# Kernel tuning notes

Measured on AMD Instinct MI355X. Metric: run time of the kernel, lower is better.

## Reference

```python
import jax, jax.numpy as jnp
import numpy as np

B, N, F = 2, 2048, 64
H, C = 4, 32          # attention heads, channels per head
HID = 128             # hidden_size
HIN = H * C           # hidden_size_in = 128
MASK = -10e9          # spektral dense-GAT mask constant


def setup_inputs() -> dict:
    key = jax.random.key(0)
    ks = jax.random.split(key, 48)
    inp = {}
    inp['x'] = jax.random.normal(ks[0], (B, N, F), dtype=jnp.float32)
    adj = (jax.random.uniform(ks[1], (B, N, N)) < 0.03).astype(jnp.float32)
    inp['a'] = jnp.clip(adj + jnp.eye(N, dtype=jnp.float32)[None], 0.0, 1.0)
    inp['h_p'] = jax.random.normal(ks[2], (B, N, HID), dtype=jnp.float32) * 0.1
    inp['h_mu'] = jax.random.normal(ks[3], (B, N, HID), dtype=jnp.float32) * 0.1
    inp['h_sigma'] = jax.random.normal(ks[4], (B, N, HID), dtype=jnp.float32) * 0.1
    # GAT params
    inp['gat_kernel'] = jax.random.normal(ks[5], (F, H, C), dtype=jnp.float32) / np.float32(np.sqrt(F))
    inp['gat_attn_self'] = jax.random.normal(ks[6], (H, C), dtype=jnp.float32) * 0.1
    inp['gat_attn_neigh'] = jax.random.normal(ks[7], (H, C), dtype=jnp.float32) * 0.1
    inp['gat_bias'] = jnp.zeros((H * C,), dtype=jnp.float32)
    # GRU-style gate params for p / mu / sigma
    ki = 8
    for nm in ('p', 'mu', 'sigma'):
        for g in ('u', 'r', 'c'):
            inp[f'W_{g}_{nm}'] = jax.random.normal(ks[ki], (HID + HIN, HID), dtype=jnp.float32) / np.float32(np.sqrt(HID + HIN)); ki += 1
            inp[f'b_{g}_{nm}'] = jax.random.normal(ks[ki], (N, 1), dtype=jnp.float32) * 0.05; ki += 1
    # bilinear decoders
    for nm in ('p', 'mu', 'sigma'):
        inp[f'R_{nm}'] = jax.random.normal(ks[ki], (HID, HID), dtype=jnp.float32) / np.float32(np.sqrt(HID)); ki += 1
    return inp


def _gat(x, a, kernel, attn_self, attn_neigh, bias):
    # dense spektral GATConv, concat_heads=True, no activation
    h = jnp.einsum('bnf,fhc->bnhc', x, kernel)                 # [B,N,H,C]
    s_self = jnp.einsum('bnhc,hc->bnh', h, attn_self)          # [B,N,H]
    s_neigh = jnp.einsum('bnhc,hc->bnh', h, attn_neigh)        # [B,N,H]
    scores = s_self[:, :, None, :] + s_neigh[:, None, :, :]    # [B,N,N,H]
    scores = jax.nn.leaky_relu(scores, negative_slope=0.2)
    scores = scores + MASK * (1.0 - a)[..., None]
    attn = jax.nn.softmax(scores, axis=2)                      # softmax over neighbors j
    out = jnp.einsum('bijh,bjhc->bihc', attn, h)               # [B,N,H,C]
    return out.reshape(out.shape[0], out.shape[1], H * C) + bias


def _gru(conv, h, Wu, Wr, Wc, bu, br, bc):
    ch = jnp.concatenate([conv, h], axis=-1)                   # [B,N,HIN+HID]
    u = jax.nn.sigmoid(bu + ch @ Wu)                           # bias [N,1] broadcasts
    r = jax.nn.sigmoid(br + ch @ Wr)
    c = jnp.tanh(bc + jnp.concatenate([conv, r * h], axis=-1) @ Wc)
    return u * h + (1.0 - u) * c


def _bilinear(h, R):
    return jnp.einsum('bnh,hk,bmk->bnm', h, R, h)              # x R x^T


def reference(x, a, h_p, h_mu, h_sigma,
              gat_kernel, gat_attn_self, gat_attn_neigh, gat_bias,
              W_u_p, b_u_p, W_r_p, b_r_p, W_c_p, b_c_p,
              W_u_mu, b_u_mu, W_r_mu, b_r_mu, W_c_mu, b_c_mu,
              W_u_sigma, b_u_sigma, W_r_sigma, b_r_sigma, W_c_sigma, b_c_sigma,
              R_p, R_mu, R_sigma):
    conv = _gat(x, a, gat_kernel, gat_attn_self, gat_attn_neigh, gat_bias)
    hp = _gru(conv, h_p, W_u_p, W_r_p, W_c_p, b_u_p, b_r_p, b_c_p)
    hmu = _gru(conv, h_mu, W_u_mu, W_r_mu, W_c_mu, b_u_mu, b_r_mu, b_c_mu)
    hsg = _gru(conv, h_sigma, W_u_sigma, W_r_sigma, W_c_sigma, b_u_sigma, b_r_sigma, b_c_sigma)
    p = _bilinear(hp, R_p)
    mu = _bilinear(hmu, R_mu)
    sigma = _bilinear(hsg, R_sigma)
    logits = jnp.stack([p, mu, sigma], axis=-1)                # [B,N,N,3]
    return logits, hp, hmu, hsg
```

## Files before the change

kernel.cpp:

```cpp
#include <hip/hip_runtime.h>
#include <hip/hip_bf16.h>

typedef __attribute__((ext_vector_type(4))) float f32x4;
typedef __attribute__((ext_vector_type(8))) short bf16x8;

static constexpr int B   = 2;
static constexpr int N   = 2048;
static constexpr int F   = 64;
static constexpr int H   = 4;
static constexpr int HID = 128;
static constexpr int BN  = B * N;
static constexpr size_t LOG_SZ = (size_t)B * N * N * 3;

__device__ __forceinline__ float sigmoidf_(float x) { return 1.0f / (1.0f + __expf(-x)); }
__device__ __forceinline__ float tanhf_(float x) {
  float e = __expf(2.0f * x);
  return 1.0f - 2.0f / (e + 1.0f);
}
__device__ __forceinline__ void split_bf16(float v, short& hi, short& lo) {
  unsigned u = __float_as_uint(v);
  unsigned hr = (u + 0x7FFFu + ((u >> 16) & 1u)) >> 16;
  hi = (short)hr;
  float hv = __uint_as_float(hr << 16);
  float res = v - hv;
  unsigned u2 = __float_as_uint(res);
  lo = (short)((u2 + 0x7FFFu + ((u2 >> 16) & 1u)) >> 16);
}

__device__ __forceinline__ void stage16(const short* gp, short* lp) {
  __builtin_amdgcn_global_load_lds(
      (const __attribute__((address_space(1))) void*)gp,
      (__attribute__((address_space(3))) void*)lp, 16, 0, 0);
}

struct PreArgs {
  const float* x; const float* gk; const float* asel; const float* anei;
  float* hfeat; float* sself; float* sneigh;
  const float* h[3];
  short* hh[3]; short* hl[3];
  const float* src[12];
  short* whi[12]; short* wlo[12];
  int nks[12];
};
__global__ __launch_bounds__(256) void k_pre(PreArgs pa) {
  const int bid = blockIdx.x;
  if (bid < BN / 2) {
    const int t = threadIdx.x;
    const int r = t >> 7, tt = t & 127;
    const int bn = bid * 2 + r;
    __shared__ float xs[2][F];
    if (tt < F) xs[r][tt] = pa.x[(size_t)bn * F + tt];
    const size_t o = (size_t)bn * HID + tt;
    { short hi, lo; split_bf16(pa.h[0][o], hi, lo); pa.hh[0][o] = hi; pa.hl[0][o] = lo; }
    { short hi, lo; split_bf16(pa.h[1][o], hi, lo); pa.hh[1][o] = hi; pa.hl[1][o] = lo; }
    { short hi, lo; split_bf16(pa.h[2][o], hi, lo); pa.hh[2][o] = hi; pa.hl[2][o] = lo; }
    __syncthreads();
    float acc = 0.f;
    #pragma unroll 8
    for (int f = 0; f < F; ++f) acc += xs[r][f] * pa.gk[f * HID + tt];
    pa.hfeat[o] = acc;
    float ps = acc * pa.asel[tt];
    float pn = acc * pa.anei[tt];
    #pragma unroll
    for (int d = 16; d >= 1; d >>= 1) {
      ps += __shfl_xor(ps, d, 32);
      pn += __shfl_xor(pn, d, 32);
    }
    if ((tt & 31) == 0) {
      pa.sself [bn * H + (tt >> 5)] = ps;
      pa.sneigh[bn * H + (tt >> 5)] = pn;
    }
  } else {
    const int pb = bid - BN / 2;
    const int m = pb >> 3, cf = pb & 7;
    const int nksv = pa.nks[m];
    const int wv = threadIdx.x >> 6, lane = threadIdx.x & 63;
    const float* src = pa.src[m];
    short* ph = pa.whi[m];
    short* pl = pa.wlo[m];
    const int col = cf * 16 + (lane & 15);
    const int krow = (lane >> 4) * 8;
    for (int ks = wv; ks < nksv; ks += 4) {
      bf16x8 vh, vl;
      #pragma unroll
      for (int e = 0; e < 8; ++e) {
        const int k = ks * 32 + krow + e;
        short hi, lo; split_bf16(src[(size_t)k * HID + col], hi, lo);
        vh[e] = hi; vl[e] = lo;
      }
      const size_t o = (((size_t)cf * nksv + ks) * 64 + lane) * 8;
      *(bf16x8*)&ph[o] = vh;
      *(bf16x8*)&pl[o] = vl;
    }
  }
}

__global__ __launch_bounds__(256) void k_attn(
    const float* __restrict__ a, const float* __restrict__ hfeat,
    const float* __restrict__ sself, const float* __restrict__ sneigh,
    const float* __restrict__ bias,
    short* __restrict__ conv_hi, short* __restrict__ conv_lo) {
  const int wv   = threadIdx.x >> 6;
  const int lane = threadIdx.x & 63;
  const int bi   = blockIdx.x * 4 + wv;
  const int bbase = bi & ~(N - 1);
  __shared__ int   nbr[4][256];
  __shared__ float wts[4][256][4];
  int*   nb       = nbr[wv];
  float (*wt)[4]  = wts[wv];

  const float si0 = sself[bi * H + 0];
  const float si1 = sself[bi * H + 1];
  const float si2 = sself[bi * H + 2];
  const float si3 = sself[bi * H + 3];
  float den0 = 0.f, den1 = 0.f, den2 = 0.f, den3 = 0.f;
  float acc0 = 0.f, acc1 = 0.f;
  const unsigned long long lmlt = ((unsigned long long)1 << lane) - 1ull;
  const float* arow = a + (size_t)bi * N;
  const float* hb   = hfeat + (size_t)bbase * HID;
  const float* snb  = sneigh + (size_t)bbase * H;
  const int h0 = lane >> 5;
  int num = 0;

  auto flush = [&]() {
    asm volatile("s_waitcnt lgkmcnt(0)" ::: "memory");
    for (int n = lane; n < num; n += 64) {
      const int j = nb[n];
      f32x4 sn = *(const f32x4*)&snb[(size_t)j * H];
      float s0 = si0 + sn[0]; s0 = (s0 > 0.f) ? s0 : 0.2f * s0;
      float s1 = si1 + sn[1]; s1 = (s1 > 0.f) ? s1 : 0.2f * s1;
      float s2 = si2 + sn[2]; s2 = (s2 > 0.f) ? s2 : 0.2f * s2;
      float s3 = si3 + sn[3]; s3 = (s3 > 0.f) ? s3 : 0.2f * s3;
      float w0 = __expf(s0), w1 = __expf(s1), w2 = __expf(s2), w3 = __expf(s3);
      wt[n][0] = w0; wt[n][1] = w1; wt[n][2] = w2; wt[n][3] = w3;
      den0 += w0; den1 += w1; den2 += w2; den3 += w3;
    }
    asm volatile("s_waitcnt lgkmcnt(0)" ::: "memory");
    #pragma unroll 4
    for (int n = 0; n < num; ++n) {
      const int j  = nb[n];
      const float wA = wt[n][h0];
      const float wB = wt[n][h0 + 2];
      const float* hr = hb + (size_t)j * HID;
      acc0 += wA * hr[lane];
      acc1 += wB * hr[lane + 64];
    }
    asm volatile("s_waitcnt lgkmcnt(0)" ::: "memory");
    num = 0;
  };

  for (int jb = 0; jb < N; jb += 256) {
    f32x4 av = *(const f32x4*)&arow[jb + lane * 4];
    #pragma unroll
    for (int e = 0; e < 4; ++e) {
      const unsigned long long m = __ballot(av[e] > 0.5f);
      if (av[e] > 0.5f) {
        const int pos = num + __popcll(m & lmlt);
        nb[pos] = jb + lane * 4 + e;
      }
      num += __popcll(m);
      if (num > 192) flush();
    }
  }
  if (num > 0) flush();

  #pragma unroll
  for (int d = 32; d >= 1; d >>= 1) {
    den0 += __shfl_xor(den0, d, 64);
    den1 += __shfl_xor(den1, d, 64);
    den2 += __shfl_xor(den2, d, 64);
    den3 += __shfl_xor(den3, d, 64);
  }
  const float dA = h0 ? den1 : den0;
  const float dB = h0 ? den3 : den2;
  const float v0 = acc0 / dA + bias[lane];
  const float v1 = acc1 / dB + bias[64 + lane];
  { short hi, lo; split_bf16(v0, hi, lo);
    conv_hi[(size_t)bi * HID + lane] = hi; conv_lo[(size_t)bi * HID + lane] = lo; }
  { short hi, lo; split_bf16(v1, hi, lo);
    conv_hi[(size_t)bi * HID + 64 + lane] = hi; conv_lo[(size_t)bi * HID + 64 + lane] = lo; }
}

struct GArgs {
  const short* chi; const short* clo;
  const float* h[3];
  const short* hhi[3]; const short* hlo[3];
  const float* bu[3]; const float* br[3]; const float* bc[3];
  const short* WuH[3]; const short* WuL[3];
  const short* WrH[3]; const short* WrL[3];
  const short* WcH[3]; const short* WcL[3];
  const short* RtH[3]; const short* RtL[3];
  float* u_ws[3];
  short* rhh[3]; short* rhl[3];
  short* hph[3]; short* hpl[3];
  float* hout[3]; __hip_bfloat16* hb[3]; __hip_bfloat16* gb[3];
};

__global__ __launch_bounds__(256) void k_ur(GArgs ga) {
  const int wv = threadIdx.x >> 6, lane = threadIdx.x & 63;
  const int bx = blockIdx.x, cg = blockIdx.y;
  const int gate = blockIdx.z & 1, cell = blockIdx.z >> 1;
  const int lr = lane & 15, lg = lane >> 4, kb = lg * 8;
  const int R0 = bx * 64 + wv * 16;
  __shared__ short wlds[2][16][64][8];

  bf16x8 a_h[8], a_l[8];
  {
    const size_t ab = (size_t)(R0 + lr) * HID + kb;
    const short* hhi = ga.hhi[cell]; const short* hlo = ga.hlo[cell];
    #pragma unroll
    for (int ks = 0; ks < 4; ++ks) {
      a_h[ks]     = *(const bf16x8*)&ga.chi[ab + ks * 32];
      a_l[ks]     = *(const bf16x8*)&ga.clo[ab + ks * 32];
      a_h[4 + ks] = *(const bf16x8*)&hhi[ab + ks * 32];
      a_l[4 + ks] = *(const bf16x8*)&hlo[ab + ks * 32];
    }
  }
  {
    const short* WH = gate ? ga.WrH[cell] : ga.WuH[cell];
    const short* WL = gate ? ga.WrL[cell] : ga.WuL[cell];
    #pragma unroll
    for (int i = 0; i < 8; ++i) {
      const int fid = wv * 8 + i;
      const int combo = fid >> 4, f = fid & 15;
      const short* src = combo ? WL : WH;
      const short* gp = src + (((size_t)((cg * 2 + (f >> 3)) * 8 + (f & 7))) * 64 + lane) * 8;
      stage16(gp, &wlds[combo][f][0][0]);
    }
  }
  asm volatile("s_waitcnt vmcnt(0)" ::: "memory");
  __syncthreads();

  f32x4 acc[2] = {};
  #pragma unroll
  for (int ks = 0; ks < 8; ++ks) {
    const bf16x8 ah = a_h[ks], al = a_l[ks];
    #pragma unroll
    for (int cfl = 0; cfl < 2; ++cfl) {
      const int f = cfl * 8 + ks;
      bf16x8 bh = *(const bf16x8*)&wlds[0][f][lane][0];
      bf16x8 bl = *(const bf16x8*)&wlds[1][f][lane][0];
      acc[cfl] = __builtin_amdgcn_mfma_f32_16x16x32_bf16(ah, bh, acc[cfl], 0, 0, 0);
      acc[cfl] = __builtin_amdgcn_mfma_f32_16x16x32_bf16(ah, bl, acc[cfl], 0, 0, 0);
      acc[cfl] = __builtin_amdgcn_mfma_f32_16x16x32_bf16(al, bh, acc[cfl], 0, 0, 0);
    }
  }
  if (gate == 0) {
    const float* bu = ga.bu[cell];
    float* uws = ga.u_ws[cell];
    #pragma unroll
    for (int cfl = 0; cfl < 2; ++cfl) {
      const int col = cg * 32 + cfl * 16 + lr;
      #pragma unroll
      for (int q = 0; q < 4; ++q) {
        const int row = R0 + lg * 4 + q;
        uws[(size_t)row * HID + col] = sigmoidf_(acc[cfl][q] + bu[row & (N - 1)]);
      }
    }
  } else {
    const float* br = ga.br[cell];
    const float* hsrc = ga.h[cell];
    short* rhh = ga.rhh[cell]; short* rhl = ga.rhl[cell];
    #pragma unroll
    for (int cfl = 0; cfl < 2; ++cfl) {
      const int col = cg * 32 + cfl * 16 + lr;
      #pragma unroll
      for (int q = 0; q < 4; ++q) {
        const int row = R0 + lg * 4 + q;
        const float rv = sigmoidf_(acc[cfl][q] + br[row & (N - 1)]);
        const float rhv = rv * hsrc[(size_t)row * HID + col];
        short hi, lo; split_bf16(rhv, hi, lo);
        rhh[(size_t)row * HID + col] = hi;
        rhl[(size_t)row * HID + col] = lo;
      }
    }
  }
}

__global__ __launch_bounds__(256) void k_c(GArgs ga) {
  const int wv = threadIdx.x >> 6, lane = threadIdx.x & 63;
  const int bx = blockIdx.x, cg = blockIdx.y, cell = blockIdx.z;
  const int lr = lane & 15, lg = lane >> 4, kb = lg * 8;
  const int R0 = bx * 64 + wv * 16;
  __shared__ short wlds[2][16][64][8];

  bf16x8 a_h[8], a_l[8];
  {
    const size_t ab = (size_t)(R0 + lr) * HID + kb;
    const short* rhh = ga.rhh[cell]; const short* rhl = ga.rhl[cell];
    #pragma unroll
    for (int ks = 0; ks < 4; ++ks) {
      a_h[ks]     = *(const bf16x8*)&ga.chi[ab + ks * 32];
      a_l[ks]     = *(const bf16x8*)&ga.clo[ab + ks * 32];
      a_h[4 + ks] = *(const bf16x8*)&rhh[ab + ks * 32];
      a_l[4 + ks] = *(const bf16x8*)&rhl[ab + ks * 32];
    }
  }
  {
    const short* WH = ga.WcH[cell];
    const short* WL = ga.WcL[cell];
    #pragma unroll
    for (int i = 0; i < 8; ++i) {
      const int fid = wv * 8 + i;
      const int combo = fid >> 4, f = fid & 15;
      const short* src = combo ? WL : WH;
      const short* gp = src + (((size_t)((cg * 2 + (f >> 3)) * 8 + (f & 7))) * 64 + lane) * 8;
      stage16(gp, &wlds[combo][f][0][0]);
    }
  }
  asm volatile("s_waitcnt vmcnt(0)" ::: "memory");
  __syncthreads();

  f32x4 acc[2] = {};
  #pragma unroll
  for (int ks = 0; ks < 8; ++ks) {
    const bf16x8 ah = a_h[ks], al = a_l[ks];
    #pragma unroll
    for (int cfl = 0; cfl < 2; ++cfl) {
      const int f = cfl * 8 + ks;
      bf16x8 bh = *(const bf16x8*)&wlds[0][f][lane][0];
      bf16x8 bl = *(const bf16x8*)&wlds[1][f][lane][0];
      acc[cfl] = __builtin_amdgcn_mfma_f32_16x16x32_bf16(ah, bh, acc[cfl], 0, 0, 0);
      acc[cfl] = __builtin_amdgcn_mfma_f32_16x16x32_bf16(ah, bl, acc[cfl], 0, 0, 0);
      acc[cfl] = __builtin_amdgcn_mfma_f32_16x16x32_bf16(al, bh, acc[cfl], 0, 0, 0);
    }
  }
  const float* bc = ga.bc[cell];
  const float* uw = ga.u_ws[cell];
  const float* hsrc = ga.h[cell];
  float* hout = ga.hout[cell];
  __hip_bfloat16* hbo = ga.hb[cell];
  short* hph = ga.hph[cell]; short* hpl = ga.hpl[cell];
  #pragma unroll
  for (int cfl = 0; cfl < 2; ++cfl) {
    const int col = cg * 32 + cfl * 16 + lr;
    #pragma unroll
    for (int q = 0; q < 4; ++q) {
      const int row = R0 + lg * 4 + q;
      const float cv = tanhf_(acc[cfl][q] + bc[row & (N - 1)]);
      const float uv = uw[(size_t)row * HID + col];
      const float hv = hsrc[(size_t)row * HID + col];
      const float o = uv * hv + (1.f - uv) * cv;
      hout[(size_t)row * HID + col] = o;
      hbo[(size_t)row * HID + col] = __float2bfloat16(o);
      short hi, lo; split_bf16(o, hi, lo);
      hph[(size_t)row * HID + col] = hi;
      hpl[(size_t)row * HID + col] = lo;
    }
  }
}

__global__ __launch_bounds__(256) void k_g(GArgs ga) {
  const int wv = threadIdx.x >> 6, lane = threadIdx.x & 63;
  const int bx = blockIdx.x, cg = blockIdx.y, cell = blockIdx.z;
  const int lr = lane & 15, lg = lane >> 4, kb = lg * 8;
  const int R0 = bx * 64 + wv * 16;
  __shared__ short wlds[2][8][64][8];

  bf16x8 a_h[4], a_l[4];
  {
    const size_t ab = (size_t)(R0 + lr) * HID + kb;
    const short* hph = ga.hph[cell]; const short* hpl = ga.hpl[cell];
    #pragma unroll
    for (int ks = 0; ks < 4; ++ks) {
      a_h[ks] = *(const bf16x8*)&hph[ab + ks * 32];
      a_l[ks] = *(const bf16x8*)&hpl[ab + ks * 32];
    }
  }
  {
    #pragma unroll
    for (int i = 0; i < 4; ++i) {
      const int fid = wv * 4 + i;
      const int combo = fid >> 3, f = fid & 7;
      const short* src = combo ? ga.RtL[cell] : ga.RtH[cell];
      const short* gp = src + (((size_t)((cg * 2 + (f >> 2)) * 4 + (f & 3))) * 64 + lane) * 8;
      stage16(gp, &wlds[combo][f][0][0]);
    }
  }
  asm volatile("s_waitcnt vmcnt(0)" ::: "memory");
  __syncthreads();

  f32x4 acc[2] = {};
  #pragma unroll
  for (int ks = 0; ks < 4; ++ks) {
    const bf16x8 ah = a_h[ks], al = a_l[ks];
    #pragma unroll
    for (int cfl = 0; cfl < 2; ++cfl) {
      const int f = cfl * 4 + ks;
      bf16x8 bh = *(const bf16x8*)&wlds[0][f][lane][0];
      bf16x8 bl = *(const bf16x8*)&wlds[1][f][lane][0];
      acc[cfl] = __builtin_amdgcn_mfma_f32_16x16x32_bf16(ah, bh, acc[cfl], 0, 0, 0);
      acc[cfl] = __builtin_amdgcn_mfma_f32_16x16x32_bf16(ah, bl, acc[cfl], 0, 0, 0);
      acc[cfl] = __builtin_amdgcn_mfma_f32_16x16x32_bf16(al, bh, acc[cfl], 0, 0, 0);
    }
  }
  __hip_bfloat16* gbo = ga.gb[cell];
  #pragma unroll
  for (int cfl = 0; cfl < 2; ++cfl) {
    const int col = cg * 32 + cfl * 16 + lr;
    #pragma unroll
    for (int q = 0; q < 4; ++q) {
      const int row = R0 + lg * 4 + q;
      gbo[(size_t)row * HID + col] = __float2bfloat16(acc[cfl][q]);
    }
  }
}

__global__ __launch_bounds__(256) void k_bilinear(
    const __hip_bfloat16* __restrict__ g0, const __hip_bfloat16* __restrict__ g1,
    const __hip_bfloat16* __restrict__ g2, const __hip_bfloat16* __restrict__ h0,
    const __hip_bfloat16* __restrict__ h1, const __hip_bfloat16* __restrict__ h2,
    float* __restrict__ out) {
  const int ti = blockIdx.x, tj = blockIdx.y, b = blockIdx.z;
  const int t = threadIdx.x;
  const int w = t >> 6, l = t & 63;
  const int wi = w >> 1, wj = w & 1;
  const int i_base = ti * 64 + wi * 32;
  const int j_base = tj * 64 + wj * 32;
  const __hip_bfloat16* gbs[3] = {g0, g1, g2};
  const __hip_bfloat16* hbs[3] = {h0, h1, h2};
  const int lr = l & 15;
  const int kb = (l >> 4) * 8;
  f32x4 acc[3][2][2] = {};
  for (int k0 = 0; k0 < HID; k0 += 32) {
    bf16x8 af[3][2], bfr[3][2];
    #pragma unroll
    for (int d = 0; d < 3; ++d) {
      #pragma unroll
      for (int m = 0; m < 2; ++m) {
        af[d][m]  = *(const bf16x8*)&gbs[d][(size_t)(b * N + i_base + m * 16 + lr) * HID + k0 + kb];
        bfr[d][m] = *(const bf16x8*)&hbs[d][(size_t)(b * N + j_base + m * 16 + lr) * HID + k0 + kb];
      }
    }
    #pragma unroll
    for (int d = 0; d < 3; ++d)
      #pragma unroll
      for (int mi = 0; mi < 2; ++mi)
        #pragma unroll
        for (int mj = 0; mj < 2; ++mj)
          acc[d][mi][mj] = __builtin_amdgcn_mfma_f32_16x16x32_bf16(
              af[d][mi], bfr[d][mj], acc[d][mi][mj], 0, 0, 0);
  }
  const int orow = (l >> 4) * 4;
  const int col  = l & 15;
  #pragma unroll
  for (int mi = 0; mi < 2; ++mi)
    #pragma unroll
    for (int mj = 0; mj < 2; ++mj)
      #pragma unroll
      for (int r = 0; r < 4; ++r) {
        const int row = i_base + mi * 16 + orow + r;
        const int cc  = j_base + mj * 16 + col;
        float* p = &out[(((size_t)(b * N + row)) * N + cc) * 3];
        p[0] = acc[0][mi][mj][r];
        p[1] = acc[1][mi][mj][r];
        p[2] = acc[2][mi][mj][r];
      }
}

extern "C" void kernel_launch(void* const* d_in, const int* in_sizes, int n_in,
                              void* d_out, int out_size, void* d_ws, size_t ws_size,
                              hipStream_t stream) {
  (void)in_sizes; (void)n_in; (void)out_size; (void)ws_size;
  const float* a    = (const float*)d_in[1];
  const float* bias = (const float*)d_in[8];

  float* ws      = (float*)d_ws;
  float* hfeat   = ws;
  float* sself   = hfeat + (size_t)BN * HID;
  float* sneigh  = sself + (size_t)BN * H;
  float* u_ws0   = sneigh + (size_t)BN * H;
  short* sp      = (short*)(u_ws0 + 3 * (size_t)BN * HID);
  auto alloc_s = [&](size_t n) { short* p = sp; sp += n; return p; };

  short* conv_hi = alloc_s((size_t)BN * HID);
  short* conv_lo = alloc_s((size_t)BN * HID);
  short* h_hi[3]; short* h_lo[3];
  for (int c = 0; c < 3; ++c) { h_hi[c] = alloc_s((size_t)BN * HID); h_lo[c] = alloc_s((size_t)BN * HID); }
  short* rh_hi[3]; short* rh_lo[3];
  for (int c = 0; c < 3; ++c) { rh_hi[c] = alloc_s((size_t)BN * HID); rh_lo[c] = alloc_s((size_t)BN * HID); }
  short* hp_hi[3]; short* hp_lo[3];
  for (int c = 0; c < 3; ++c) { hp_hi[c] = alloc_s((size_t)BN * HID); hp_lo[c] = alloc_s((size_t)BN * HID); }
  __hip_bfloat16* hbb[3]; __hip_bfloat16* gbb[3];
  for (int c = 0; c < 3; ++c) {
    hbb[c] = (__hip_bfloat16*)alloc_s((size_t)BN * HID);
    gbb[c] = (__hip_bfloat16*)alloc_s((size_t)BN * HID);
  }

  float* out = (float*)d_out;

  PreArgs pa;
  pa.x = (const float*)d_in[0];
  pa.gk = (const float*)d_in[5];
  pa.asel = (const float*)d_in[6];
  pa.anei = (const float*)d_in[7];
  pa.hfeat = hfeat; pa.sself = sself; pa.sneigh = sneigh;

  GArgs ga;
  ga.chi = conv_hi; ga.clo = conv_lo;
  ga.h[0] = (const float*)d_in[2];
  ga.h[1] = (const float*)d_in[3];
  ga.h[2] = (const float*)d_in[4];
  for (int c = 0; c < 3; ++c) {
    pa.h[c] = ga.h[c];
    pa.hh[c] = h_hi[c]; pa.hl[c] = h_lo[c];
    const int base = 9 + c * 6;
    ga.hhi[c] = h_hi[c]; ga.hlo[c] = h_lo[c];
    ga.bu[c] = (const float*)d_in[base + 1];
    ga.br[c] = (const float*)d_in[base + 3];
    ga.bc[c] = (const float*)d_in[base + 5];
    short* wu_h = alloc_s(256 * 128); short* wu_l = alloc_s(256 * 128);
    short* wr_h = alloc_s(256 * 128); short* wr_l = alloc_s(256 * 128);
    short* wc_h = alloc_s(256 * 128); short* wc_l = alloc_s(256 * 128);
    short* rt_h = alloc_s(128 * 128); short* rt_l = alloc_s(128 * 128);
    const int pb = c * 4;
    pa.src[pb + 0] = (const float*)d_in[base + 0]; pa.whi[pb + 0] = wu_h; pa.wlo[pb + 0] = wu_l; pa.nks[pb + 0] = 8;
    pa.src[pb + 1] = (const float*)d_in[base + 2]; pa.whi[pb + 1] = wr_h; pa.wlo[pb + 1] = wr_l; pa.nks[pb + 1] = 8;
    pa.src[pb + 2] = (const float*)d_in[base + 4]; pa.whi[pb + 2] = wc_h; pa.wlo[pb + 2] = wc_l; pa.nks[pb + 2] = 8;
    pa.src[pb + 3] = (const float*)d_in[27 + c];   pa.whi[pb + 3] = rt_h; pa.wlo[pb + 3] = rt_l; pa.nks[pb + 3] = 4;
    ga.WuH[c] = wu_h; ga.WuL[c] = wu_l;
    ga.WrH[c] = wr_h; ga.WrL[c] = wr_l;
    ga.WcH[c] = wc_h; ga.WcL[c] = wc_l;
    ga.RtH[c] = rt_h; ga.RtL[c] = rt_l;
    ga.u_ws[c] = u_ws0 + (size_t)c * BN * HID;
    ga.rhh[c] = rh_hi[c]; ga.rhl[c] = rh_lo[c];
    ga.hph[c] = hp_hi[c]; ga.hpl[c] = hp_lo[c];
    ga.hout[c] = out + LOG_SZ + (size_t)c * BN * HID;
    ga.hb[c] = hbb[c];
    ga.gb[c] = gbb[c];
  }

  k_pre<<<BN / 2 + 96, 256, 0, stream>>>(pa);
  k_attn<<<BN / 4, 256, 0, stream>>>(a, hfeat, sself, sneigh, bias, conv_hi, conv_lo);
  k_ur<<<dim3(BN / 64, 4, 6), 256, 0, stream>>>(ga);
  k_c<<<dim3(BN / 64, 4, 3), 256, 0, stream>>>(ga);
  k_g<<<dim3(BN / 64, 4, 3), 256, 0, stream>>>(ga);
  dim3 g2(N / 64, N / 64, B);
  k_bilinear<<<g2, 256, 0, stream>>>(gbb[0], gbb[1], gbb[2],
                                     hbb[0], hbb[1], hbb[2], out);
}
```

Baseline: 116.3 us.

## Fuse all stages into one cooperative persistent megakernel with grid syncs

```diff
diff --git a/kernel.cpp b/kernel.cpp
--- a/kernel.cpp
+++ b/kernel.cpp
@@ -1,5 +1,8 @@
 #include <hip/hip_runtime.h>
 #include <hip/hip_bf16.h>
+#include <hip/hip_cooperative_groups.h>
+
+namespace cg = cooperative_groups;
 
 typedef __attribute__((ext_vector_type(4))) float f32x4;
 typedef __attribute__((ext_vector_type(8))) short bf16x8;
@@ -26,11 +29,428 @@
   unsigned u2 = __float_as_uint(res);
   lo = (short)((u2 + 0x7FFFu + ((u2 >> 16) & 1u)) >> 16);
 }
-
 __device__ __forceinline__ void stage16(const short* gp, short* lp) {
   __builtin_amdgcn_global_load_lds(
       (const __attribute__((address_space(1))) void*)gp,
       (__attribute__((address_space(3))) void*)lp, 16, 0, 0);
+}
+
+struct MegaArgs {
+  const float* x; const float* gk; const float* asel; const float* anei;
+  const float* a; const float* bias;
+  float* hfeat; float* sself; float* sneigh;
+  const float* h[3];
+  short* hh[3]; short* hl[3];
+  const float* wsrc[12];
+  short* whi[12]; short* wlo[12];
+  short* conv_hi; short* conv_lo;
+  const float* bu[3]; const float* br[3]; const float* bc[3];
+  const short* WuH[3]; const short* WuL[3];
+  const short* WrH[3]; const short* WrL[3];
+  const short* WcH[3]; const short* WcL[3];
+  const short* RtH[3]; const short* RtL[3];
+  float* u_ws[3];
+  short* rhh[3]; short* rhl[3];
+  short* hph[3]; short* hpl[3];
+  float* hout[3];
+  short* gb[3];
+  float* out;
+};
+
+__global__ __launch_bounds__(512, 4) void k_mega(MegaArgs A) {
+  cg::grid_group grid = cg::this_grid();
+  const int blk = blockIdx.x;
+  const int G   = gridDim.x;
+  const int t   = threadIdx.x;
+  const int wv  = t >> 6, lane = t & 63;
+  __shared__ char smem[65536];
+
+  {
+    float (*xs)[64] = (float (*)[64])smem;
+    const int sub = t >> 7, tt = t & 127;
+    for (int r0 = blk * 4; r0 < BN; r0 += G * 4) {
+      const int r = r0 + sub;
+      if (tt < 64) xs[sub][tt] = A.x[(size_t)r * F + tt];
+      const size_t o = (size_t)r * HID + tt;
+      { short hi, lo; split_bf16(A.h[0][o], hi, lo); A.hh[0][o] = hi; A.hl[0][o] = lo; }
+      { short hi, lo; split_bf16(A.h[1][o], hi, lo); A.hh[1][o] = hi; A.hl[1][o] = lo; }
+      { short hi, lo; split_bf16(A.h[2][o], hi, lo); A.hh[2][o] = hi; A.hl[2][o] = lo; }
+      __syncthreads();
+      float acc = 0.f;
+      #pragma unroll 8
+      for (int f = 0; f < F; ++f) acc += xs[sub][f] * A.gk[f * HID + tt];
+      A.hfeat[o] = acc;
+      float ps = acc * A.asel[tt];
+      float pn = acc * A.anei[tt];
+      #pragma unroll
+      for (int d = 16; d >= 1; d >>= 1) {
+        ps += __shfl_xor(ps, d, 32);
+        pn += __shfl_xor(pn, d, 32);
+      }
+      if ((tt & 31) == 0) {
+        A.sself [r * H + (tt >> 5)] = ps;
+        A.sneigh[r * H + (tt >> 5)] = pn;
+      }
+      __syncthreads();
+    }
+    for (int u = blk * 8 + wv; u < 672; u += G * 8) {
+      const int c = u / 224, rem = u % 224;
+      int m, cf, ks, nks;
+      if (rem < 192) { m = c * 4 + rem / 64; const int f2 = rem & 63; cf = f2 >> 3; ks = f2 & 7; nks = 8; }
+      else           { m = c * 4 + 3;        const int f2 = rem - 192; cf = f2 >> 2; ks = f2 & 3; nks = 4; }
+      const float* src = A.wsrc[m];
+      short* ph = A.whi[m];
+      short* pl = A.wlo[m];
+      const int col  = cf * 16 + (lane & 15);
+      const int krow = (lane >> 4) * 8;
+      bf16x8 vh, vl;
+      #pragma unroll
+      for (int e = 0; e < 8; ++e) {
+        short hi, lo; split_bf16(src[(size_t)(ks * 32 + krow + e) * HID + col], hi, lo);
+        vh[e] = hi; vl[e] = lo;
+      }
+      const size_t o = (((size_t)cf * nks + ks) * 64 + lane) * 8;
+      *(bf16x8*)&ph[o] = vh;
+      *(bf16x8*)&pl[o] = vl;
+    }
+  }
+  grid.sync();
+
+  {
+    int   (*nbrA)[256]    = (int (*)[256])smem;
+    float (*wtsA)[256][4] = (float (*)[256][4])(smem + 8192);
+    const unsigned long long lmlt = ((unsigned long long)1 << lane) - 1ull;
+    const int h0 = lane >> 5;
+    for (int bi = blk * 8 + wv; bi < BN; bi += G * 8) {
+      int*   nb      = nbrA[wv];
+      float (*wt)[4] = wtsA[wv];
+      const int bbase = bi & ~(N - 1);
+      const float si0 = A.sself[bi * H + 0];
+      const float si1 = A.sself[bi * H + 1];
+      const float si2 = A.sself[bi * H + 2];
+      const float si3 = A.sself[bi * H + 3];
+      float den0 = 0.f, den1 = 0.f, den2 = 0.f, den3 = 0.f;
+      float acc0 = 0.f, acc1 = 0.f;
+      const float* arow = A.a + (size_t)bi * N;
+      const float* hb   = A.hfeat + (size_t)bbase * HID;
+      const float* snb  = A.sneigh + (size_t)bbase * H;
+      int num = 0;
+
+      auto flush = [&]() {
+        asm volatile("s_waitcnt lgkmcnt(0)" ::: "memory");
+        for (int n = lane; n < num; n += 64) {
+          const int j = nb[n];
+          f32x4 sn = *(const f32x4*)&snb[(size_t)j * H];
+          float s0 = si0 + sn[0]; s0 = (s0 > 0.f) ? s0 : 0.2f * s0;
+          float s1 = si1 + sn[1]; s1 = (s1 > 0.f) ? s1 : 0.2f * s1;
+          float s2 = si2 + sn[2]; s2 = (s2 > 0.f) ? s2 : 0.2f * s2;
+          float s3 = si3 + sn[3]; s3 = (s3 > 0.f) ? s3 : 0.2f * s3;
+          float w0 = __expf(s0), w1 = __expf(s1), w2 = __expf(s2), w3 = __expf(s3);
+          wt[n][0] = w0; wt[n][1] = w1; wt[n][2] = w2; wt[n][3] = w3;
+          den0 += w0; den1 += w1; den2 += w2; den3 += w3;
+        }
+        asm volatile("s_waitcnt lgkmcnt(0)" ::: "memory");
+        #pragma unroll 4
+        for (int n = 0; n < num; ++n) {
+          const int j  = nb[n];
+          const float wA = wt[n][h0];
+          const float wB = wt[n][h0 + 2];
+          const float* hr = hb + (size_t)j * HID;
+          acc0 += wA * hr[lane];
+          acc1 += wB * hr[lane + 64];
+        }
+        asm volatile("s_waitcnt lgkmcnt(0)" ::: "memory");
+        num = 0;
+      };
+
+      for (int jb = 0; jb < N; jb += 256) {
+        f32x4 av = *(const f32x4*)&arow[jb + lane * 4];
+        #pragma unroll
+        for (int e = 0; e < 4; ++e) {
+          const unsigned long long m = __ballot(av[e] > 0.5f);
+          if (av[e] > 0.5f) {
+            const int pos = num + __popcll(m & lmlt);
+            nb[pos] = jb + lane * 4 + e;
+          }
+          num += __popcll(m);
+          if (num > 192) flush();
+        }
+      }
+      if (num > 0) flush();
+
+      #pragma unroll
+      for (int d = 32; d >= 1; d >>= 1) {
+        den0 += __shfl_xor(den0, d, 64);
+        den1 += __shfl_xor(den1, d, 64);
+        den2 += __shfl_xor(den2, d, 64);
+        den3 += __shfl_xor(den3, d, 64);
+      }
+      const float dA = h0 ? den1 : den0;
+      const float dB = h0 ? den3 : den2;
+      const float v0 = acc0 / dA + A.bias[lane];
+      const float v1 = acc1 / dB + A.bias[64 + lane];
+      { short hi, lo; split_bf16(v0, hi, lo);
+        A.conv_hi[(size_t)bi * HID + lane] = hi; A.conv_lo[(size_t)bi * HID + lane] = lo; }
+      { short hi, lo; split_bf16(v1, hi, lo);
+        A.conv_hi[(size_t)bi * HID + 64 + lane] = hi; A.conv_lo[(size_t)bi * HID + 64 + lane] = lo; }
+    }
+  }
+  grid.sync();
+
+  {
+    short (*wlds)[16][64][8] = (short (*)[16][64][8])smem;
+    const int lr = lane & 15, lg = lane >> 4, kb = lg * 8;
+    for (int vb = blk; vb < 384; vb += G) {
+      const int cell = vb >> 7, rem = vb & 127;
+      const int cgp = rem & 3, rb = rem >> 2;
+      const int R0 = rb * 128 + wv * 16;
+      bf16x8 a_h[8], a_l[8];
+      {
+        const size_t ab = (size_t)(R0 + lr) * HID + kb;
+        const short* hhi = A.hh[cell]; const short* hlo = A.hl[cell];
+        #pragma unroll
+        for (int ks = 0; ks < 4; ++ks) {
+          a_h[ks]     = *(const bf16x8*)&A.conv_hi[ab + ks * 32];
+          a_l[ks]     = *(const bf16x8*)&A.conv_lo[ab + ks * 32];
+          a_h[4 + ks] = *(const bf16x8*)&hhi[ab + ks * 32];
+          a_l[4 + ks] = *(const bf16x8*)&hlo[ab + ks * 32];
+        }
+      }
+      {
+        const short* srcs[4] = { A.WuH[cell], A.WuL[cell], A.WrH[cell], A.WrL[cell] };
+        #pragma unroll
+        for (int i = 0; i < 8; ++i) {
+          const int fid = wv * 8 + i;
+          const int combo = fid >> 4, f = fid & 15;
+          const short* gp = srcs[combo] +
+              (((size_t)((cgp * 2 + (f >> 3)) * 8 + (f & 7))) * 64 + lane) * 8;
+          stage16(gp, &wlds[combo][f][0][0]);
+        }
+      }
+      asm volatile("s_waitcnt vmcnt(0)" ::: "memory");
+      __syncthreads();
+
+      f32x4 au[2] = {}, ar[2] = {};
+      #pragma unroll
+      for (int ks = 0; ks < 8; ++ks) {
+        const bf16x8 ah = a_h[ks], al = a_l[ks];
+        #pragma unroll
+        for (int cfl = 0; cfl < 2; ++cfl) {
+          const int f = cfl * 8 + ks;
+          bf16x8 buh = *(const bf16x8*)&wlds[0][f][lane][0];
+          bf16x8 bul = *(const bf16x8*)&wlds[1][f][lane][0];
+          bf16x8 brh = *(const bf16x8*)&wlds[2][f][lane][0];
+          bf16x8 brl = *(const bf16x8*)&wlds[3][f][lane][0];
+          au[cfl] = __builtin_amdgcn_mfma_f32_16x16x32_bf16(ah, buh, au[cfl], 0, 0, 0);
+          au[cfl] = __builtin_amdgcn_mfma_f32_16x16x32_bf16(ah, bul, au[cfl], 0, 0, 0);
+          au[cfl] = __builtin_amdgcn_mfma_f32_16x16x32_bf16(al, buh, au[cfl], 0, 0, 0);
+          ar[cfl] = __builtin_amdgcn_mfma_f32_16x16x32_bf16(ah, brh, ar[cfl], 0, 0, 0);
+          ar[cfl] = __builtin_amdgcn_mfma_f32_16x16x32_bf16(ah, brl, ar[cfl], 0, 0, 0);
+          ar[cfl] = __builtin_amdgcn_mfma_f32_16x16x32_bf16(al, brh, ar[cfl], 0, 0, 0);
+        }
+      }
+      const float* bu = A.bu[cell];
+      const float* br = A.br[cell];
+      const float* hsrc = A.h[cell];
+      float* uws = A.u_ws[cell];
+      short* rhh = A.rhh[cell]; short* rhl = A.rhl[cell];
+      #pragma unroll
+      for (int cfl = 0; cfl < 2; ++cfl) {
+        const int col = cgp * 32 + cfl * 16 + lr;
+        #pragma unroll
+        for (int q = 0; q < 4; ++q) {
+          const int row = R0 + lg * 4 + q;
+          const int n = row & (N - 1);
+          uws[(size_t)row * HID + col] = sigmoidf_(au[cfl][q] + bu[n]);
+          const float rv = sigmoidf_(ar[cfl][q] + br[n]);
+          const float rhv = rv * hsrc[(size_t)row * HID + col];
+          short hi, lo; split_bf16(rhv, hi, lo);
+          rhh[(size_t)row * HID + col] = hi;
+          rhl[(size_t)row * HID + col] = lo;
+        }
+      }
+      __syncthreads();
+    }
+  }
+  grid.sync();
+
+  {
+    short (*wlds)[16][64][8] = (short (*)[16][64][8])smem;
+    const int lr = lane & 15, lg = lane >> 4, kb = lg * 8;
+    for (int vb = blk; vb < 384; vb += G) {
+      const int cell = vb >> 7, rem = vb & 127;
+      const int cgp = rem & 3, rb = rem >> 2;
+      const int R0 = rb * 128 + wv * 16;
+      bf16x8 a_h[8], a_l[8];
+      {
+        const size_t ab = (size_t)(R0 + lr) * HID + kb;
+        const short* rhh = A.rhh[cell]; const short* rhl = A.rhl[cell];
+        #pragma unroll
+        for (int ks = 0; ks < 4; ++ks) {
+          a_h[ks]     = *(const bf16x8*)&A.conv_hi[ab + ks * 32];
+          a_l[ks]     = *(const bf16x8*)&A.conv_lo[ab + ks * 32];
+          a_h[4 + ks] = *(const bf16x8*)&rhh[ab + ks * 32];
+          a_l[4 + ks] = *(const bf16x8*)&rhl[ab + ks * 32];
+        }
+      }
+      {
+        const short* srcs[2] = { A.WcH[cell], A.WcL[cell] };
+        #pragma unroll
+        for (int i = 0; i < 4; ++i) {
+          const int fid = wv * 4 + i;
+          const int combo = fid >> 4, f = fid & 15;
+          const short* gp = srcs[combo] +
+              (((size_t)((cgp * 2 + (f >> 3)) * 8 + (f & 7))) * 64 + lane) * 8;
+          stage16(gp, &wlds[combo][f][0][0]);
+        }
+      }
+      asm volatile("s_waitcnt vmcnt(0)" ::: "memory");
+      __syncthreads();
+
+      f32x4 acc[2] = {};
+      #pragma unroll
+      for (int ks = 0; ks < 8; ++ks) {
+        const bf16x8 ah = a_h[ks], al = a_l[ks];
+        #pragma unroll
+        for (int cfl = 0; cfl < 2; ++cfl) {
+          const int f = cfl * 8 + ks;
+          bf16x8 bh = *(const bf16x8*)&wlds[0][f][lane][0];
+          bf16x8 bl = *(const bf16x8*)&wlds[1][f][lane][0];
+          acc[cfl] = __builtin_amdgcn_mfma_f32_16x16x32_bf16(ah, bh, acc[cfl], 0, 0, 0);
+          acc[cfl] = __builtin_amdgcn_mfma_f32_16x16x32_bf16(ah, bl, acc[cfl], 0, 0, 0);
+          acc[cfl] = __builtin_amdgcn_mfma_f32_16x16x32_bf16(al, bh, acc[cfl], 0, 0, 0);
+        }
+      }
+      const float* bc = A.bc[cell];
+      const float* uw = A.u_ws[cell];
+      const float* hsrc = A.h[cell];
+      float* hout = A.hout[cell];
+      short* hph = A.hph[cell]; short* hpl = A.hpl[cell];
+      #pragma unroll
+      for (int cfl = 0; cfl < 2; ++cfl) {
+        const int col = cgp * 32 + cfl * 16 + lr;
+        #pragma unroll
+        for (int q = 0; q < 4; ++q) {
+          const int row = R0 + lg * 4 + q;
+          const float cv = tanhf_(acc[cfl][q] + bc[row & (N - 1)]);
+          const float uv = uw[(size_t)row * HID + col];
+          const float hv = hsrc[(size_t)row * HID + col];
+          const float o = uv * hv + (1.f - uv) * cv;
+          __builtin_nontemporal_store(o, &hout[(size_t)row * HID + col]);
+          short hi, lo; split_bf16(o, hi, lo);
+          hph[(size_t)row * HID + col] = hi;
+          hpl[(size_t)row * HID + col] = lo;
+        }
+      }
+      __syncthreads();
+    }
+  }
+  grid.sync();
+
+  {
+    short (*wlds)[8][64][8] = (short (*)[8][64][8])smem;
+    const int lr = lane & 15, lg = lane >> 4, kb = lg * 8;
+    for (int vb = blk; vb < 384; vb += G) {
+      const int cell = vb >> 7, rem = vb & 127;
+      const int cgp = rem & 3, rb = rem >> 2;
+      const int R0 = rb * 128 + wv * 16;
+      bf16x8 a_h[4], a_l[4];
+      {
+        const size_t ab = (size_t)(R0 + lr) * HID + kb;
+        const short* hph = A.hph[cell]; const short* hpl = A.hpl[cell];
+        #pragma unroll
+        for (int ks = 0; ks < 4; ++ks) {
+          a_h[ks] = *(const bf16x8*)&hph[ab + ks * 32];
+          a_l[ks] = *(const bf16x8*)&hpl[ab + ks * 32];
+        }
+      }
+      {
+        const short* srcs[2] = { A.RtH[cell], A.RtL[cell] };
+        #pragma unroll
+        for (int i = 0; i < 2; ++i) {
+          const int fid = wv * 2 + i;
+          const int combo = fid >> 3, f = fid & 7;
+          const short* gp = srcs[combo] +
+              (((size_t)((cgp * 2 + (f >> 2)) * 4 + (f & 3))) * 64 + lane) * 8;
+          stage16(gp, &wlds[combo][f][0][0]);
+        }
+      }
+      asm volatile("s_waitcnt vmcnt(0)" ::: "memory");
+      __syncthreads();
+
+      f32x4 acc[2] = {};
+      #pragma unroll
+      for (int ks = 0; ks < 4; ++ks) {
+        const bf16x8 ah = a_h[ks], al = a_l[ks];
+        #pragma unroll
+        for (int cfl = 0; cfl < 2; ++cfl) {
+          const int f = cfl * 4 + ks;
+          bf16x8 bh = *(const bf16x8*)&wlds[0][f][lane][0];
+          bf16x8 bl = *(const bf16x8*)&wlds[1][f][lane][0];
+          acc[cfl] = __builtin_amdgcn_mfma_f32_16x16x32_bf16(ah, bh, acc[cfl], 0, 0, 0);
+          acc[cfl] = __builtin_amdgcn_mfma_f32_16x16x32_bf16(ah, bl, acc[cfl], 0, 0, 0);
+          acc[cfl] = __builtin_amdgcn_mfma_f32_16x16x32_bf16(al, bh, acc[cfl], 0, 0, 0);
+        }
+      }
+      short* gbo = A.gb[cell];
+      #pragma unroll
+      for (int cfl = 0; cfl < 2; ++cfl) {
+        const int col = cgp * 32 + cfl * 16 + lr;
+        #pragma unroll
+        for (int q = 0; q < 4; ++q) {
+          const int row = R0 + lg * 4 + q;
+          short hi, lo; split_bf16(acc[cfl][q], hi, lo);
+          gbo[(size_t)row * HID + col] = hi;
+        }
+      }
+      __syncthreads();
+    }
+  }
+  grid.sync();
+
+  {
+    const int wi = wv >> 1, wj = wv & 1;
+    const int lr = lane & 15;
+    const int kb = (lane >> 4) * 8;
+    for (int u = blk; u < 1024; u += G) {
+      const int b = u >> 9, r = u & 511;
+      const int id2 = (r & 7) * 64 + (r >> 3);
+      const int ti = id2 & 15, tj = id2 >> 4;
+      const int i_base = ti * 128 + wi * 32;
+      const int j_base = tj * 64 + wj * 32;
+      f32x4 acc[3][2][2] = {};
+      for (int k0 = 0; k0 < HID; k0 += 32) {
+        #pragma unroll
+        for (int d = 0; d < 3; ++d) {
+          const short* gsrc = A.gb[d];
+          const short* hsrc = A.hph[d];
+          bf16x8 af0 = *(const bf16x8*)&gsrc[(size_t)(b * N + i_base + lr) * HID + k0 + kb];
+          bf16x8 af1 = *(const bf16x8*)&gsrc[(size_t)(b * N + i_base + 16 + lr) * HID + k0 + kb];
+          bf16x8 bf0 = *(const bf16x8*)&hsrc[(size_t)(b * N + j_base + lr) * HID + k0 + kb];
+          bf16x8 bf1 = *(const bf16x8*)&hsrc[(size_t)(b * N + j_base + 16 + lr) * HID + k0 + kb];
+          acc[d][0][0] = __builtin_amdgcn_mfma_f32_16x16x32_bf16(af0, bf0, acc[d][0][0], 0, 0, 0);
+          acc[d][0][1] = __builtin_amdgcn_mfma_f32_16x16x32_bf16(af0, bf1, acc[d][0][1], 0, 0, 0);
+          acc[d][1][0] = __builtin_amdgcn_mfma_f32_16x16x32_bf16(af1, bf0, acc[d][1][0], 0, 0, 0);
+          acc[d][1][1] = __builtin_amdgcn_mfma_f32_16x16x32_bf16(af1, bf1, acc[d][1][1], 0, 0, 0);
+        }
+      }
+      const int orow = (lane >> 4) * 4;
+      const int col  = lane & 15;
+      #pragma unroll
+      for (int mi = 0; mi < 2; ++mi)
+        #pragma unroll
+        for (int mj = 0; mj < 2; ++mj)
+          #pragma unroll
+          for (int rr = 0; rr < 4; ++rr) {
+            const int row = i_base + mi * 16 + orow + rr;
+            const int cc  = j_base + mj * 16 + col;
+            float* p = &A.out[(((size_t)(b * N + row)) * N + cc) * 3];
+            __builtin_nontemporal_store(acc[0][mi][mj][rr], p + 0);
+            __builtin_nontemporal_store(acc[1][mi][mj][rr], p + 1);
+            __builtin_nontemporal_store(acc[2][mi][mj][rr], p + 2);
+          }
+    }
+  }
 }
 
 struct PreArgs {
@@ -108,7 +528,6 @@
   __shared__ float wts[4][256][4];
   int*   nb       = nbr[wv];
   float (*wt)[4]  = wts[wv];
-
   const float si0 = sself[bi * H + 0];
   const float si1 = sself[bi * H + 1];
   const float si2 = sself[bi * H + 2];
@@ -121,7 +540,6 @@
   const float* snb  = sneigh + (size_t)bbase * H;
   const int h0 = lane >> 5;
   int num = 0;
-
   auto flush = [&]() {
     asm volatile("s_waitcnt lgkmcnt(0)" ::: "memory");
     for (int n = lane; n < num; n += 64) {
@@ -148,7 +566,6 @@
     asm volatile("s_waitcnt lgkmcnt(0)" ::: "memory");
     num = 0;
   };
-
   for (int jb = 0; jb < N; jb += 256) {
     f32x4 av = *(const f32x4*)&arow[jb + lane * 4];
     #pragma unroll
@@ -163,7 +580,6 @@
     }
   }
   if (num > 0) flush();
-
   #pragma unroll
   for (int d = 32; d >= 1; d >>= 1) {
     den0 += __shfl_xor(den0, d, 64);
@@ -193,17 +609,15 @@
   float* u_ws[3];
   short* rhh[3]; short* rhl[3];
   short* hph[3]; short* hpl[3];
-  float* hout[3]; __hip_bfloat16* hb[3]; __hip_bfloat16* gb[3];
+  float* hout[3]; short* gb[3];
 };
 
 __global__ __launch_bounds__(256) void k_ur(GArgs ga) {
   const int wv = threadIdx.x >> 6, lane = threadIdx.x & 63;
-  const int bx = blockIdx.x, cg = blockIdx.y;
-  const int gate = blockIdx.z & 1, cell = blockIdx.z >> 1;
+  const int bx = blockIdx.x, cg2 = blockIdx.y, cell = blockIdx.z;
   const int lr = lane & 15, lg = lane >> 4, kb = lg * 8;
   const int R0 = bx * 64 + wv * 16;
-  __shared__ short wlds[2][16][64][8];
-
+  __shared__ short wlds[4][16][64][8];
   bf16x8 a_h[8], a_l[8];
   {
     const size_t ab = (size_t)(R0 + lr) * HID + kb;
@@ -217,20 +631,89 @@
     }
   }
   {
-    const short* WH = gate ? ga.WrH[cell] : ga.WuH[cell];
-    const short* WL = gate ? ga.WrL[cell] : ga.WuL[cell];
+    const short* srcs[4] = { ga.WuH[cell], ga.WuL[cell], ga.WrH[cell], ga.WrL[cell] };
+    const short* sp = srcs[wv];
+    #pragma unroll
+    for (int f = 0; f < 16; ++f) {
+      const short* gp = sp + (((size_t)((cg2 * 2 + (f >> 3)) * 8 + (f & 7))) * 64 + lane) * 8;
+      stage16(gp, &wlds[wv][f][0][0]);
+    }
+  }
+  asm volatile("s_waitcnt vmcnt(0)" ::: "memory");
+  __syncthreads();
+  f32x4 au[2] = {}, ar[2] = {};
+  #pragma unroll
+  for (int ks = 0; ks < 8; ++ks) {
+    const bf16x8 ah = a_h[ks], al = a_l[ks];
+    #pragma unroll
+    for (int cfl = 0; cfl < 2; ++cfl) {
+      const int f = cfl * 8 + ks;
+      bf16x8 buh = *(const bf16x8*)&wlds[0][f][lane][0];
+      bf16x8 bul = *(const bf16x8*)&wlds[1][f][lane][0];
+      bf16x8 brh = *(const bf16x8*)&wlds[2][f][lane][0];
+      bf16x8 brl = *(const bf16x8*)&wlds[3][f][lane][0];
+      au[cfl] = __builtin_amdgcn_mfma_f32_16x16x32_bf16(ah, buh, au[cfl], 0, 0, 0);
+      au[cfl] = __builtin_amdgcn_mfma_f32_16x16x32_bf16(ah, bul, au[cfl], 0, 0, 0);
+      au[cfl] = __builtin_amdgcn_mfma_f32_16x16x32_bf16(al, buh, au[cfl], 0, 0, 0);
+      ar[cfl] = __builtin_amdgcn_mfma_f32_16x16x32_bf16(ah, brh, ar[cfl], 0, 0, 0);
+      ar[cfl] = __builtin_amdgcn_mfma_f32_16x16x32_bf16(ah, brl, ar[cfl], 0, 0, 0);
+      ar[cfl] = __builtin_amdgcn_mfma_f32_16x16x32_bf16(al, brh, ar[cfl], 0, 0, 0);
+    }
+  }
+  const float* bu = ga.bu[cell];
+  const float* br = ga.br[cell];
+  const float* hsrc = ga.h[cell];
+  float* uws = ga.u_ws[cell];
+  short* rhh = ga.rhh[cell]; short* rhl = ga.rhl[cell];
+  #pragma unroll
+  for (int cfl = 0; cfl < 2; ++cfl) {
+    const int col = cg2 * 32 + cfl * 16 + lr;
+    #pragma unroll
+    for (int q = 0; q < 4; ++q) {
+      const int row = R0 + lg * 4 + q;
+      const int n = row & (N - 1);
+      uws[(size_t)row * HID + col] = sigmoidf_(au[cfl][q] + bu[n]);
+      const float rv = sigmoidf_(ar[cfl][q] + br[n]);
+      const float rhv = rv * hsrc[(size_t)row * HID + col];
+      short hi, lo; split_bf16(rhv, hi, lo);
+      rhh[(size_t)row * HID + col] = hi;
+      rhl[(size_t)row * HID + col] = lo;
+    }
+  }
+}
+
+__global__ __launch_bounds__(256) void k_c(GArgs ga) {
+  const int wv = threadIdx.x >> 6, lane = threadIdx.x & 63;
+  const int bx = blockIdx.x, cg2 = blockIdx.y, cell = blockIdx.z;
+  const int lr = lane & 15, lg = lane >> 4, kb = lg * 8;
+  const int R0 = bx * 64 + wv * 16;
+  __shared__ short wlds[2][16][64][8];
+  bf16x8 a_h[8], a_l[8];
+  {
+    const size_t ab = (size_t)(R0 + lr) * HID + kb;
+    const short* rhh = ga.rhh[cell]; const short* rhl = ga.rhl[cell];
+    #pragma unroll
+    for (int ks = 0; ks < 4; ++ks) {
+      a_h[ks]     = *(const bf16x8*)&ga.chi[ab + ks * 32];
+      a_l[ks]     = *(const bf16x8*)&ga.clo[ab + ks * 32];
+      a_h[4 + ks] = *(const bf16x8*)&rhh[ab + ks * 32];
+      a_l[4 + ks] = *(const bf16x8*)&rhl[ab + ks * 32];
+    }
+  }
+  {
+    const short* WH = ga.WcH[cell];
+    const short* WL = ga.WcL[cell];
     #pragma unroll
     for (int i = 0; i < 8; ++i) {
       const int fid = wv * 8 + i;
       const int combo = fid >> 4, f = fid & 15;
       const short* src = combo ? WL : WH;
-      const short* gp = src + (((size_t)((cg * 2 + (f >> 3)) * 8 + (f & 7))) * 64 + lane) * 8;
+      const short* gp = src + (((size_t)((cg2 * 2 + (f >> 3)) * 8 + (f & 7))) * 64 + lane) * 8;
       stage16(gp, &wlds[combo][f][0][0]);
     }
   }
   asm volatile("s_waitcnt vmcnt(0)" ::: "memory");
   __syncthreads();
-
   f32x4 acc[2] = {};
   #pragma unroll
   for (int ks = 0; ks < 8; ++ks) {
@@ -245,95 +728,14 @@
       acc[cfl] = __builtin_amdgcn_mfma_f32_16x16x32_bf16(al, bh, acc[cfl], 0, 0, 0);
     }
   }
-  if (gate == 0) {
-    const float* bu = ga.bu[cell];
-    float* uws = ga.u_ws[cell];
-    #pragma unroll
-    for (int cfl = 0; cfl < 2; ++cfl) {
-      const int col = cg * 32 + cfl * 16 + lr;
-      #pragma unroll
-      for (int q = 0; q < 4; ++q) {
-        const int row = R0 + lg * 4 + q;
-        uws[(size_t)row * HID + col] = sigmoidf_(acc[cfl][q] + bu[row & (N - 1)]);
-      }
-    }
-  } else {
-    const float* br = ga.br[cell];
-    const float* hsrc = ga.h[cell];
-    short* rhh = ga.rhh[cell]; short* rhl = ga.rhl[cell];
-    #pragma unroll
-    for (int cfl = 0; cfl < 2; ++cfl) {
-      const int col = cg * 32 + cfl * 16 + lr;
-      #pragma unroll
-      for (int q = 0; q < 4; ++q) {
-        const int row = R0 + lg * 4 + q;
-        const float rv = sigmoidf_(acc[cfl][q] + br[row & (N - 1)]);
-        const float rhv = rv * hsrc[(size_t)row * HID + col];
-        short hi, lo; split_bf16(rhv, hi, lo);
-        rhh[(size_t)row * HID + col] = hi;
-        rhl[(size_t)row * HID + col] = lo;
-      }
-    }
-  }
-}
-
-__global__ __launch_bounds__(256) void k_c(GArgs ga) {
-  const int wv = threadIdx.x >> 6, lane = threadIdx.x & 63;
-  const int bx = blockIdx.x, cg = blockIdx.y, cell = blockIdx.z;
-  const int lr = lane & 15, lg = lane >> 4, kb = lg * 8;
-  const int R0 = bx * 64 + wv * 16;
-  __shared__ short wlds[2][16][64][8];
-
-  bf16x8 a_h[8], a_l[8];
-  {
-    const size_t ab = (size_t)(R0 + lr) * HID + kb;
-    const short* rhh = ga.rhh[cell]; const short* rhl = ga.rhl[cell];
-    #pragma unroll
-    for (int ks = 0; ks < 4; ++ks) {
-      a_h[ks]     = *(const bf16x8*)&ga.chi[ab + ks * 32];
-      a_l[ks]     = *(const bf16x8*)&ga.clo[ab + ks * 32];
-      a_h[4 + ks] = *(const bf16x8*)&rhh[ab + ks * 32];
-      a_l[4 + ks] = *(const bf16x8*)&rhl[ab + ks * 32];
-    }
-  }
-  {
-    const short* WH = ga.WcH[cell];
-    const short* WL = ga.WcL[cell];
-    #pragma unroll
-    for (int i = 0; i < 8; ++i) {
-      const int fid = wv * 8 + i;
-      const int combo = fid >> 4, f = fid & 15;
-      const short* src = combo ? WL : WH;
-      const short* gp = src + (((size_t)((cg * 2 + (f >> 3)) * 8 + (f & 7))) * 64 + lane) * 8;
-      stage16(gp, &wlds[combo][f][0][0]);
-    }
-  }
-  asm volatile("s_waitcnt vmcnt(0)" ::: "memory");
-  __syncthreads();
-
-  f32x4 acc[2] = {};
-  #pragma unroll
-  for (int ks = 0; ks < 8; ++ks) {
-    const bf16x8 ah = a_h[ks], al = a_l[ks];
-    #pragma unroll
-    for (int cfl = 0; cfl < 2; ++cfl) {
-      const int f = cfl * 8 + ks;
-      bf16x8 bh = *(const bf16x8*)&wlds[0][f][lane][0];
-      bf16x8 bl = *(const bf16x8*)&wlds[1][f][lane][0];
-      acc[cfl] = __builtin_amdgcn_mfma_f32_16x16x32_bf16(ah, bh, acc[cfl], 0, 0, 0);
-      acc[cfl] = __builtin_amdgcn_mfma_f32_16x16x32_bf16(ah, bl, acc[cfl], 0, 0, 0);
-      acc[cfl] = __builtin_amdgcn_mfma_f32_16x16x32_bf16(al, bh, acc[cfl], 0, 0, 0);
-    }
-  }
   const float* bc = ga.bc[cell];
   const float* uw = ga.u_ws[cell];
   const float* hsrc = ga.h[cell];
   float* hout = ga.hout[cell];
-  __hip_bfloat16* hbo = ga.hb[cell];
   short* hph = ga.hph[cell]; short* hpl = ga.hpl[cell];
   #pragma unroll
   for (int cfl = 0; cfl < 2; ++cfl) {
-    const int col = cg * 32 + cfl * 16 + lr;
+    const int col = cg2 * 32 + cfl * 16 + lr;
     #pragma unroll
     for (int q = 0; q < 4; ++q) {
       const int row = R0 + lg * 4 + q;
@@ -341,8 +743,7 @@
       const float uv = uw[(size_t)row * HID + col];
       const float hv = hsrc[(size_t)row * HID + col];
       const float o = uv * hv + (1.f - uv) * cv;
-      hout[(size_t)row * HID + col] = o;
-      hbo[(size_t)row * HID + col] = __float2bfloat16(o);
+      __builtin_nontemporal_store(o, &hout[(size_t)row * HID + col]);
       short hi, lo; split_bf16(o, hi, lo);
       hph[(size_t)row * HID + col] = hi;
       hpl[(size_t)row * HID + col] = lo;
@@ -352,11 +753,10 @@
 
 __global__ __launch_bounds__(256) void k_g(GArgs ga) {
   const int wv = threadIdx.x >> 6, lane = threadIdx.x & 63;
-  const int bx = blockIdx.x, cg = blockIdx.y, cell = blockIdx.z;
+  const int bx = blockIdx.x, cg2 = blockIdx.y, cell = blockIdx.z;
   const int lr = lane & 15, lg = lane >> 4, kb = lg * 8;
   const int R0 = bx * 64 + wv * 16;
   __shared__ short wlds[2][8][64][8];
-
   bf16x8 a_h[4], a_l[4];
   {
     const size_t ab = (size_t)(R0 + lr) * HID + kb;
@@ -373,13 +773,12 @@
       const int fid = wv * 4 + i;
       const int combo = fid >> 3, f = fid & 7;
       const short* src = combo ? ga.RtL[cell] : ga.RtH[cell];
-      const short* gp = src + (((size_t)((cg * 2 + (f >> 2)) * 4 + (f & 3))) * 64 + lane) * 8;
+      const short* gp = src + (((size_t)((cg2 * 2 + (f >> 2)) * 4 + (f & 3))) * 64 + lane) * 8;
       stage16(gp, &wlds[combo][f][0][0]);
     }
   }
   asm volatile("s_waitcnt vmcnt(0)" ::: "memory");
   __syncthreads();
-
   f32x4 acc[2] = {};
   #pragma unroll
   for (int ks = 0; ks < 4; ++ks) {
@@ -394,52 +793,50 @@
       acc[cfl] = __builtin_amdgcn_mfma_f32_16x16x32_bf16(al, bh, acc[cfl], 0, 0, 0);
     }
   }
-  __hip_bfloat16* gbo = ga.gb[cell];
+  short* gbo = ga.gb[cell];
   #pragma unroll
   for (int cfl = 0; cfl < 2; ++cfl) {
-    const int col = cg * 32 + cfl * 16 + lr;
+    const int col = cg2 * 32 + cfl * 16 + lr;
     #pragma unroll
     for (int q = 0; q < 4; ++q) {
       const int row = R0 + lg * 4 + q;
-      gbo[(size_t)row * HID + col] = __float2bfloat16(acc[cfl][q]);
-    }
-  }
-}
-
-__global__ __launch_bounds__(256) void k_bilinear(
-    const __hip_bfloat16* __restrict__ g0, const __hip_bfloat16* __restrict__ g1,
-    const __hip_bfloat16* __restrict__ g2, const __hip_bfloat16* __restrict__ h0,
-    const __hip_bfloat16* __restrict__ h1, const __hip_bfloat16* __restrict__ h2,
+      short hi, lo; split_bf16(acc[cfl][q], hi, lo);
+      gbo[(size_t)row * HID + col] = hi;
+    }
+  }
+}
+
+__global__ __launch_bounds__(512) void k_bilinear(
+    const short* __restrict__ g0, const short* __restrict__ g1,
+    const short* __restrict__ g2, const short* __restrict__ h0,
+    const short* __restrict__ h1, const short* __restrict__ h2,
     float* __restrict__ out) {
-  const int ti = blockIdx.x, tj = blockIdx.y, b = blockIdx.z;
+  const int id  = blockIdx.y * 16 + blockIdx.x;
+  const int id2 = (id & 7) * 64 + (id >> 3);
+  const int ti = id2 & 15, tj = id2 >> 4;
+  const int b = blockIdx.z;
   const int t = threadIdx.x;
   const int w = t >> 6, l = t & 63;
   const int wi = w >> 1, wj = w & 1;
-  const int i_base = ti * 64 + wi * 32;
+  const int i_base = ti * 128 + wi * 32;
   const int j_base = tj * 64 + wj * 32;
-  const __hip_bfloat16* gbs[3] = {g0, g1, g2};
-  const __hip_bfloat16* hbs[3] = {h0, h1, h2};
+  const short* gbs[3] = {g0, g1, g2};
+  const short* hbs[3] = {h0, h1, h2};
   const int lr = l & 15;
   const int kb = (l >> 4) * 8;
   f32x4 acc[3][2][2] = {};
   for (int k0 = 0; k0 < HID; k0 += 32) {
-    bf16x8 af[3][2], bfr[3][2];
     #pragma unroll
     for (int d = 0; d < 3; ++d) {
-      #pragma unroll
-      for (int m = 0; m < 2; ++m) {
-        af[d][m]  = *(const bf16x8*)&gbs[d][(size_t)(b * N + i_base + m * 16 + lr) * HID + k0 + kb];
-        bfr[d][m] = *(const bf16x8*)&hbs[d][(size_t)(b * N + j_base + m * 16 + lr) * HID + k0 + kb];
-      }
-    }
-    #pragma unroll
-    for (int d = 0; d < 3; ++d)
-      #pragma unroll
-      for (int mi = 0; mi < 2; ++mi)
-        #pragma unroll
-        for (int mj = 0; mj < 2; ++mj)
-          acc[d][mi][mj] = __builtin_amdgcn_mfma_f32_16x16x32_bf16(
-              af[d][mi], bfr[d][mj], acc[d][mi][mj], 0, 0, 0);
+      bf16x8 af0 = *(const bf16x8*)&gbs[d][(size_t)(b * N + i_base + lr) * HID + k0 + kb];
+      bf16x8 af1 = *(const bf16x8*)&gbs[d][(size_t)(b * N + i_base + 16 + lr) * HID + k0 + kb];
+      bf16x8 bf0 = *(const bf16x8*)&hbs[d][(size_t)(b * N + j_base + lr) * HID + k0 + kb];
+      bf16x8 bf1 = *(const bf16x8*)&hbs[d][(size_t)(b * N + j_base + 16 + lr) * HID + k0 + kb];
+      acc[d][0][0] = __builtin_amdgcn_mfma_f32_16x16x32_bf16(af0, bf0, acc[d][0][0], 0, 0, 0);
+      acc[d][0][1] = __builtin_amdgcn_mfma_f32_16x16x32_bf16(af0, bf1, acc[d][0][1], 0, 0, 0);
+      acc[d][1][0] = __builtin_amdgcn_mfma_f32_16x16x32_bf16(af1, bf0, acc[d][1][0], 0, 0, 0);
+      acc[d][1][1] = __builtin_amdgcn_mfma_f32_16x16x32_bf16(af1, bf1, acc[d][1][1], 0, 0, 0);
+    }
   }
   const int orow = (l >> 4) * 4;
   const int col  = l & 15;
@@ -452,9 +849,9 @@
         const int row = i_base + mi * 16 + orow + r;
         const int cc  = j_base + mj * 16 + col;
         float* p = &out[(((size_t)(b * N + row)) * N + cc) * 3];
-        p[0] = acc[0][mi][mj][r];
-        p[1] = acc[1][mi][mj][r];
-        p[2] = acc[2][mi][mj][r];
+        __builtin_nontemporal_store(acc[0][mi][mj][r], p + 0);
+        __builtin_nontemporal_store(acc[1][mi][mj][r], p + 1);
+        __builtin_nontemporal_store(acc[2][mi][mj][r], p + 2);
       }
 }
 
@@ -462,9 +859,6 @@
                               void* d_out, int out_size, void* d_ws, size_t ws_size,
                               hipStream_t stream) {
   (void)in_sizes; (void)n_in; (void)out_size; (void)ws_size;
-  const float* a    = (const float*)d_in[1];
-  const float* bias = (const float*)d_in[8];
-
   float* ws      = (float*)d_ws;
   float* hfeat   = ws;
   float* sself   = hfeat + (size_t)BN * HID;
@@ -481,61 +875,98 @@
   for (int c = 0; c < 3; ++c) { rh_hi[c] = alloc_s((size_t)BN * HID); rh_lo[c] = alloc_s((size_t)BN * HID); }
   short* hp_hi[3]; short* hp_lo[3];
   for (int c = 0; c < 3; ++c) { hp_hi[c] = alloc_s((size_t)BN * HID); hp_lo[c] = alloc_s((size_t)BN * HID); }
-  __hip_bfloat16* hbb[3]; __hip_bfloat16* gbb[3];
+  short* gbb[3];
+  for (int c = 0; c < 3; ++c) gbb[c] = alloc_s((size_t)BN * HID);
+
+  float* out = (float*)d_out;
+
+  MegaArgs ma;
+  ma.x = (const float*)d_in[0];
+  ma.a = (const float*)d_in[1];
+  ma.gk = (const float*)d_in[5];
+  ma.asel = (const float*)d_in[6];
+  ma.anei = (const float*)d_in[7];
+  ma.bias = (const float*)d_in[8];
+  ma.hfeat = hfeat; ma.sself = sself; ma.sneigh = sneigh;
+  ma.conv_hi = conv_hi; ma.conv_lo = conv_lo;
+  ma.out = out;
+  ma.h[0] = (const float*)d_in[2];
+  ma.h[1] = (const float*)d_in[3];
+  ma.h[2] = (const float*)d_in[4];
   for (int c = 0; c < 3; ++c) {
-    hbb[c] = (__hip_bfloat16*)alloc_s((size_t)BN * HID);
-    gbb[c] = (__hip_bfloat16*)alloc_s((size_t)BN * HID);
-  }
-
-  float* out = (float*)d_out;
-
-  PreArgs pa;
-  pa.x = (const float*)d_in[0];
-  pa.gk = (const float*)d_in[5];
-  pa.asel = (const float*)d_in[6];
-  pa.anei = (const float*)d_in[7];
-  pa.hfeat = hfeat; pa.sself = sself; pa.sneigh = sneigh;
-
-  GArgs ga;
-  ga.chi = conv_hi; ga.clo = conv_lo;
-  ga.h[0] = (const float*)d_in[2];
-  ga.h[1] = (const float*)d_in[3];
-  ga.h[2] = (const float*)d_in[4];
-  for (int c = 0; c < 3; ++c) {
-    pa.h[c] = ga.h[c];
-    pa.hh[c] = h_hi[c]; pa.hl[c] = h_lo[c];
     const int base = 9 + c * 6;
-    ga.hhi[c] = h_hi[c]; ga.hlo[c] = h_lo[c];
-    ga.bu[c] = (const float*)d_in[base + 1];
-    ga.br[c] = (const float*)d_in[base + 3];
-    ga.bc[c] = (const float*)d_in[base + 5];
+    ma.hh[c] = h_hi[c]; ma.hl[c] = h_lo[c];
+    ma.bu[c] = (const float*)d_in[base + 1];
+    ma.br[c] = (const float*)d_in[base + 3];
+    ma.bc[c] = (const float*)d_in[base + 5];
     short* wu_h = alloc_s(256 * 128); short* wu_l = alloc_s(256 * 128);
     short* wr_h = alloc_s(256 * 128); short* wr_l = alloc_s(256 * 128);
     short* wc_h = alloc_s(256 * 128); short* wc_l = alloc_s(256 * 128);
     short* rt_h = alloc_s(128 * 128); short* rt_l = alloc_s(128 * 128);
     const int pb = c * 4;
-    pa.src[pb + 0] = (const float*)d_in[base + 0]; pa.whi[pb + 0] = wu_h; pa.wlo[pb + 0] = wu_l; pa.nks[pb + 0] = 8;
-    pa.src[pb + 1] = (const float*)d_in[base + 2]; pa.whi[pb + 1] = wr_h; pa.wlo[pb + 1] = wr_l; pa.nks[pb + 1] = 8;
-    pa.src[pb + 2] = (const float*)d_in[base + 4]; pa.whi[pb + 2] = wc_h; pa.wlo[pb + 2] = wc_l; pa.nks[pb + 2] = 8;
-    pa.src[pb + 3] = (const float*)d_in[27 + c];   pa.whi[pb + 3] = rt_h; pa.wlo[pb + 3] = rt_l; pa.nks[pb + 3] = 4;
-    ga.WuH[c] = wu_h; ga.WuL[c] = wu_l;
-    ga.WrH[c] = wr_h; ga.WrL[c] = wr_l;
-    ga.WcH[c] = wc_h; ga.WcL[c] = wc_l;
-    ga.RtH[c] = rt_h; ga.RtL[c] = rt_l;
-    ga.u_ws[c] = u_ws0 + (size_t)c * BN * HID;
-    ga.rhh[c] = rh_hi[c]; ga.rhl[c] = rh_lo[c];
-    ga.hph[c] = hp_hi[c]; ga.hpl[c] = hp_lo[c];
-    ga.hout[c] = out + LOG_SZ + (size_t)c * BN * HID;
-    ga.hb[c] = hbb[c];
-    ga.gb[c] = gbb[c];
-  }
-
-  k_pre<<<BN / 2 + 96, 256, 0, stream>>>(pa);
-  k_attn<<<BN / 4, 256, 0, stream>>>(a, hfeat, sself, sneigh, bias, conv_hi, conv_lo);
-  k_ur<<<dim3(BN / 64, 4, 6), 256, 0, stream>>>(ga);
-  k_c<<<dim3(BN / 64, 4, 3), 256, 0, stream>>>(ga);
-  k_g<<<dim3(BN / 64, 4, 3), 256, 0, stream>>>(ga);
-  dim3 g2(N / 64, N / 64, B);
-  k_bilinear<<<g2, 256, 0, stream>>>(gbb[0], gbb[1], gbb[2],
-                                     hbb[0], hbb[1], hbb[2], out);
-}
+    ma.wsrc[pb + 0] = (const float*)d_in[base + 0]; ma.whi[pb + 0] = wu_h; ma.wlo[pb + 0] = wu_l;
+    ma.wsrc[pb + 1] = (const float*)d_in[base + 2]; ma.whi[pb + 1] = wr_h; ma.wlo[pb + 1] = wr_l;
+    ma.wsrc[pb + 2] = (const float*)d_in[base + 4]; ma.whi[pb + 2] = wc_h; ma.wlo[pb + 2] = wc_l;
+    ma.wsrc[pb + 3] = (const float*)d_in[27 + c];   ma.whi[pb + 3] = rt_h; ma.wlo[pb + 3] = rt_l;
+    ma.WuH[c] = wu_h; ma.WuL[c] = wu_l;
+    ma.WrH[c] = wr_h; ma.WrL[c] = wr_l;
+    ma.WcH[c] = wc_h; ma.WcL[c] = wc_l;
+    ma.RtH[c] = rt_h; ma.RtL[c] = rt_l;
+    ma.u_ws[c] = u_ws0 + (size_t)c * BN * HID;
+    ma.rhh[c] = rh_hi[c]; ma.rhl[c] = rh_lo[c];
+    ma.hph[c] = hp_hi[c]; ma.hpl[c] = hp_lo[c];
+    ma.hout[c] = out + LOG_SZ + (size_t)c * BN * HID;
+    ma.gb[c] = gbb[c];
+  }
+
+  int blocksPerCU = 0;
+  hipError_t oerr = hipOccupancyMaxActiveBlocksPerMultiprocessor(&blocksPerCU, k_mega, 512, 0);
+  int grid = 0;
+  if (oerr == hipSuccess && blocksPerCU >= 1) {
+    const int cap = blocksPerCU * 256;
+    grid = (cap >= 512) ? 512 : (cap >= 256 ? 256 : 128);
+  }
+  bool done = false;
+  if (grid > 0) {
+    void* kargs[] = { (void*)&ma };
+    hipError_t lerr = hipLaunchCooperativeKernel((const void*)k_mega, dim3(grid), dim3(512),
+                                                 kargs, 0, stream);
+    if (lerr == hipSuccess) done = true;
+  }
+
+  if (!done) {
+    PreArgs pa;
+    pa.x = ma.x; pa.gk = ma.gk; pa.asel = ma.asel; pa.anei = ma.anei;
+    pa.hfeat = hfeat; pa.sself = sself; pa.sneigh = sneigh;
+    GArgs ga;
+    ga.chi = conv_hi; ga.clo = conv_lo;
+    for (int c = 0; c < 3; ++c) {
+      pa.h[c] = ma.h[c]; pa.hh[c] = h_hi[c]; pa.hl[c] = h_lo[c];
+      ga.h[c] = ma.h[c];
+      ga.hhi[c] = h_hi[c]; ga.hlo[c] = h_lo[c];
+      ga.bu[c] = ma.bu[c]; ga.br[c] = ma.br[c]; ga.bc[c] = ma.bc[c];
+      ga.WuH[c] = ma.WuH[c]; ga.WuL[c] = ma.WuL[c];
+      ga.WrH[c] = ma.WrH[c]; ga.WrL[c] = ma.WrL[c];
+      ga.WcH[c] = ma.WcH[c]; ga.WcL[c] = ma.WcL[c];
+      ga.RtH[c] = ma.RtH[c]; ga.RtL[c] = ma.RtL[c];
+      ga.u_ws[c] = ma.u_ws[c];
+      ga.rhh[c] = rh_hi[c]; ga.rhl[c] = rh_lo[c];
+      ga.hph[c] = hp_hi[c]; ga.hpl[c] = hp_lo[c];
+      ga.hout[c] = ma.hout[c];
+      ga.gb[c] = gbb[c];
+      const int pb = c * 4;
+      pa.src[pb + 0] = ma.wsrc[pb + 0]; pa.whi[pb + 0] = ma.whi[pb + 0]; pa.wlo[pb + 0] = ma.wlo[pb + 0]; pa.nks[pb + 0] = 8;
+      pa.src[pb + 1] = ma.wsrc[pb + 1]; pa.whi[pb + 1] = ma.whi[pb + 1]; pa.wlo[pb + 1] = ma.wlo[pb + 1]; pa.nks[pb + 1] = 8;
+      pa.src[pb + 2] = ma.wsrc[pb + 2]; pa.whi[pb + 2] = ma.whi[pb + 2]; pa.wlo[pb + 2] = ma.wlo[pb + 2]; pa.nks[pb + 2] = 8;
+      pa.src[pb + 3] = ma.wsrc[pb + 3]; pa.whi[pb + 3] = ma.whi[pb + 3]; pa.wlo[pb + 3] = ma.wlo[pb + 3]; pa.nks[pb + 3] = 4;
+    }
+    k_pre<<<BN / 2 + 96, 256, 0, stream>>>(pa);
+    k_attn<<<BN / 4, 256, 0, stream>>>(ma.a, hfeat, sself, sneigh, ma.bias, conv_hi, conv_lo);
+    k_ur<<<dim3(BN / 64, 4, 3), 256, 0, stream>>>(ga);
+    k_c<<<dim3(BN / 64, 4, 3), 256, 0, stream>>>(ga);
+    k_g<<<dim3(BN / 64, 4, 3), 256, 0, stream>>>(ga);
+    dim3 g2(N / 128, N / 64, B);
+    k_bilinear<<<g2, 512, 0, stream>>>(gbb[0], gbb[1], gbb[2],
+                                       hp_hi[0], hp_hi[1], hp_hi[2], out);
+  }
+}
```

Result: slower. 307.0 us (+163.9%).
